# Optimization experiments

Hardware: AMD Instinct MI355X
Metric: run time of the kernel (lower is better)

The kernel has to match this reference:

```python
import jax, jax.numpy as jnp
import numpy as np

NT = 34000      # nodes per type
NTYPES = 3
NMP = 2         # metapaths per node type
E = 300000      # metapath instances per metapath
L = 3           # metapath length
H = 8           # attention heads
D = 64          # hidden_dim (per-head dim)
HD = H * D      # 512
AV = 128        # attn_vec_dim
C = 8           # out_dim (classes)
NTGT = 1000
NLAYERS = 2
N = NTYPES * NT


def _glorot(k, shape, fan_in):
    return jax.random.normal(k, shape, jnp.float32) * (1.0 / np.sqrt(fan_in))


def setup_inputs() -> dict:
    key = jax.random.key(0)
    ks = jax.random.split(key, 24)
    X0 = jax.random.normal(ks[0], (NT, 512), jnp.float32)
    X1 = jax.random.normal(ks[1], (NT, 256), jnp.float32)
    X2 = jax.random.normal(ks[2], (NT, 128), jnp.float32)
    # metapath instances: column 0 is the target node (must be of type i),
    # remaining columns are intermediate nodes of any type
    dst = jax.random.randint(ks[3], (NTYPES, NMP, E), 0, NT) + jnp.arange(NTYPES)[:, None, None] * NT
    mids = jax.random.randint(ks[4], (NTYPES, NMP, E, L - 1), 0, N)
    mp_idx = jnp.concatenate([dst[..., None], mids], axis=-1).astype(jnp.int32)
    target_idx = jax.random.randint(ks[5], (NTGT,), 0, NT).astype(jnp.int32)
    inp = {
        "X0": X0, "X1": X1, "X2": X2,
        # per-type feature transforms (fc_list)
        "fcW0": _glorot(ks[6], (512, D), 512), "fcb0": jnp.zeros((D,), jnp.float32),
        "fcW1": _glorot(ks[7], (256, D), 256), "fcb1": jnp.zeros((D,), jnp.float32),
        "fcW2": _glorot(ks[8], (128, D), 128), "fcb2": jnp.zeros((D,), jnp.float32),
        # GAT-style intra-metapath attention params [layer, type, metapath, H, D]
        "attn1": jax.random.normal(ks[9], (NLAYERS, NTYPES, NMP, H, D), jnp.float32) * 0.1,
        "attn2": jax.random.normal(ks[10], (NLAYERS, NTYPES, NMP, H, D), jnp.float32) * 0.1,
        # inter-metapath attention (fc1 + attention vector q) [layer, type, ...]
        "mpW": _glorot(ks[11], (NLAYERS, NTYPES, HD, AV), HD),
        "mpb": jnp.zeros((NLAYERS, NTYPES, AV), jnp.float32),
        "mpq": jax.random.normal(ks[12], (NLAYERS, NTYPES, AV), jnp.float32) * 0.1,
        # per-layer output fc: in_dim*num_heads -> out_dim
        "lW0": _glorot(ks[13], (HD, D), HD), "lb0": jnp.zeros((D,), jnp.float32),
        "lW1": _glorot(ks[14], (HD, C), HD), "lb1": jnp.zeros((C,), jnp.float32),
        "mp_idx": mp_idx,
        "target_idx": target_idx,
    }
    return inp


def _ctr_layer(h, a1, a2, mpW, mpb, mpq, mp_idx):
    # one MAGNN_nc_layer ctr-ntype pass: gather metapath instances, intra-metapath
    # attention (segment softmax over target node), inter-metapath attention,
    # then scatter per-type results into the shared node tensor (contiguous blocks).
    outs = []
    for i in range(NTYPES):
        per_mp = []
        for p in range(NMP):
            idx = mp_idx[i, p]                      # [E, L]
            feats = h[idx]                          # [E, L, D] irregular gather
            hid = feats.mean(axis=1)                # rnn_type='average' metapath encoding
            dst = idx[:, 0] - i * NT                # local target-node ids
            e = jax.nn.leaky_relu(
                jnp.einsum('ed,hd->eh', feats[:, 0, :], a1[i, p])
                + jnp.einsum('ed,hd->eh', hid, a2[i, p]), 0.2)   # [E, H]
            m = jax.ops.segment_max(e, dst, num_segments=NT)
            ex = jnp.exp(e - m[dst])
            den = jax.ops.segment_sum(ex, dst, num_segments=NT)
            alpha = ex / jnp.maximum(den[dst], 1e-9)             # segment softmax
            out = jax.ops.segment_sum(alpha[:, :, None] * hid[:, None, :], dst,
                                      num_segments=NT)           # [NT, H, D]
            per_mp.append(jax.nn.elu(out.reshape(NT, HD)))
        st = jnp.stack(per_mp)                       # [P, NT, HD]
        s = jnp.tanh(jnp.einsum('pnd,dk->pnk', st, mpW[i]) + mpb[i]).mean(axis=1) @ mpq[i]  # [P]
        beta = jax.nn.softmax(s)
        outs.append(jnp.einsum('p,pnd->nd', beta, st))
    return jnp.concatenate(outs, axis=0)             # scatter back: [N, HD]


def reference(X0, X1, X2, fcW0, fcb0, fcW1, fcb1, fcW2, fcb2,
              attn1, attn2, mpW, mpb, mpq, lW0, lb0, lW1, lb1,
              mp_idx, target_idx):
    # type-masked gather -> per-type linear -> scatter (types are contiguous blocks)
    h = jnp.concatenate([X0 @ fcW0 + fcb0, X1 @ fcW1 + fcb1, X2 @ fcW2 + fcb2], axis=0)
    hm = _ctr_layer(h, attn1[0], attn2[0], mpW[0], mpb[0], mpq[0], mp_idx)
    h = jax.nn.elu(hm @ lW0 + lb0)                   # layer 0: HD -> hidden, ELU
    hm = _ctr_layer(h, attn1[1], attn2[1], mpW[1], mpb[1], mpq[1], mp_idx)
    logits = hm @ lW1 + lb1                          # final layer: HD -> out_dim
    return logits[target_idx]
```

## Files before the change

kernel.cpp:

```cpp
#include <hip/hip_runtime.h>
#include <hip/hip_bf16.h>
#include <math.h>

#define NT 34000
#define NTYPES 3
#define NMP 2
#define NE 300000
#define HH 8
#define DD 64
#define HD 512
#define AV 128
#define NCLS 8
#define NTGT 1000
#define NN (NTYPES*NT)
#define NBLK 133
#define SCBLK 1172
#define TSC (6*SCBLK)
#define TMM (3*532)
#define MAXC 8

typedef short short8 __attribute__((ext_vector_type(8)));
typedef float f32x4 __attribute__((ext_vector_type(4)));

__device__ __forceinline__ short f2bf(float f){
  unsigned u = __float_as_uint(f);
  unsigned r = u + 0x7FFFu + ((u>>16)&1u);
  return (short)(r>>16);
}
__device__ __forceinline__ float bf2f(short s){
  return __uint_as_float(((unsigned)(unsigned short)s)<<16);
}
__device__ __forceinline__ float fast_tanh(float x){
  x = fminf(15.f, fmaxf(-15.f, x));
  float t = __expf(2.f*x);
  return (t-1.f)/(t+1.f);
}

__device__ __forceinline__ void compute_beta(const float* __restrict__ av,
                                             const float* __restrict__ q,
                                             float* b0, float* b1){
  float s0=0.f, s1=0.f;
  #pragma unroll
  for(int c=0;c<32;c++){
    float4 a0=((const float4*)av)[c];
    float4 a1=((const float4*)(av+128))[c];
    float4 qq=((const float4*)q)[c];
    s0 += a0.x*qq.x+a0.y*qq.y+a0.z*qq.z+a0.w*qq.w;
    s1 += a1.x*qq.x+a1.y*qq.y+a1.z*qq.z+a1.w*qq.w;
  }
  s0 /= (float)NT; s1 /= (float)NT;
  float mm=fmaxf(s0,s1);
  float e0=__expf(s0-mm), e1=__expf(s1-mm);
  float d=e0+e1;
  *b0=e0/d; *b1=e1/d;
}

__global__ void k_zero(int* __restrict__ p, int n){
  int i = blockIdx.x*256+threadIdx.x; if(i<n) p[i]=0;
}

__global__ void k_hist(const int* __restrict__ mp, int* __restrict__ counts){
  int e = blockIdx.x*256+threadIdx.x; int g = blockIdx.y;
  if(e>=NE) return;
  int i = g>>1;
  int dst = mp[((size_t)g*NE+e)*3] - i*NT;
  atomicAdd(&counts[g*NT+dst],1);
}

__global__ __launch_bounds__(256) void k_blkred(const int* __restrict__ counts, int* __restrict__ bsum){
  int g=blockIdx.y, blk=blockIdx.x, t=threadIdx.x;
  int idx=blk*256+t;
  int v=(idx<NT)? counts[g*NT+idx]:0;
  #pragma unroll
  for(int off=32;off;off>>=1) v+=__shfl_down(v,off,64);
  __shared__ int sh[4];
  if((t&63)==0) sh[t>>6]=v;
  __syncthreads();
  if(t==0) bsum[g*NBLK+blk]=sh[0]+sh[1]+sh[2]+sh[3];
}

__global__ __launch_bounds__(256) void k_scansums(int* __restrict__ bsum){
  int g=blockIdx.x; int t=threadIdx.x;
  __shared__ int s[256];
  int v=(t<NBLK)? bsum[g*NBLK+t]:0;
  s[t]=v; __syncthreads();
  for(int off=1;off<256;off<<=1){
    int tmp=(t>=off)?s[t-off]:0; __syncthreads();
    s[t]+=tmp; __syncthreads();
  }
  if(t<NBLK) bsum[g*NBLK+t]=s[t]-v;
}

__global__ __launch_bounds__(256) void k_scanapply(int* __restrict__ counts, const int* __restrict__ bsum,
                                                   int* __restrict__ offs){
  int g=blockIdx.y, blk=blockIdx.x, t=threadIdx.x;
  int idx=blk*256+t;
  int v=(idx<NT)? counts[g*NT+idx]:0;
  __shared__ int s[256];
  s[t]=v; __syncthreads();
  for(int off=1;off<256;off<<=1){
    int tmp=(t>=off)?s[t-off]:0; __syncthreads();
    s[t]+=tmp; __syncthreads();
  }
  int excl = s[t]-v + bsum[g*NBLK+blk];
  if(idx<NT){ offs[g*(NT+1)+idx]=excl; counts[g*NT+idx]=0; }
  if(idx==NT-1) offs[g*(NT+1)+NT]=excl+v;
}

__global__ void k_packWall(const float* __restrict__ W0, const float* __restrict__ W1,
                           const float* __restrict__ W2, const float* __restrict__ WL,
                           const float* __restrict__ mpW,
                           short* __restrict__ p0, short* __restrict__ p1,
                           short* __restrict__ p2, short* __restrict__ pL,
                           short* __restrict__ bpk4, float* __restrict__ accv){
  int which = blockIdx.y;
  int tid = blockIdx.x*256+threadIdx.x;
  if(which<4){
    const float* W; short* wpk; int K;
    if(which==0){W=W0;wpk=p0;K=512;}
    else if(which==1){W=W1;wpk=p1;K=256;}
    else if(which==2){W=W2;wpk=p2;K=128;}
    else {W=WL;wpk=pL;K=512;}
    int nk = K>>5;
    int total = nk*256;
    if(tid>=total) return;
    int lane = tid&63; int c=(tid>>6)&3; int kt=tid>>8;
    int col = c*16 + (lane&15);
    int kbase = kt*32 + ((lane>>4)<<3);
    short8 hi, lo;
    #pragma unroll
    for(int j=0;j<8;j++){
      float w = W[(size_t)(kbase+j)*64+col];
      short h = f2bf(w); hi[j]=h;
      lo[j] = f2bf(w - bf2f(h));
    }
    ((short8*)wpk)[tid] = hi;
    ((short8*)wpk)[total+tid] = lo;
  } else {
    if(which==4 && tid<1024) accv[tid]=0.f;
    if(tid>=8192) return;
    const float* W = mpW + (size_t)(which-4)*512*128;
    short* out = bpk4 + (size_t)(which-4)*65536;
    int lane=tid&63; int c=(tid>>6)&7; int t=tid>>9;
    int kbase = t*32 + ((lane>>4)<<3);
    int col = c*16 + (lane&15);
    short8 v;
    #pragma unroll
    for(int jj=0;jj<8;jj++) v[jj]=f2bf(W[(size_t)(kbase+jj)*128+col]);
    ((short8*)out)[tid]=v;
  }
}

__global__ __launch_bounds__(256) void k_scmm(const int* __restrict__ mp, const int* __restrict__ offs,
    int* __restrict__ counts, int2* __restrict__ mids,
    const float* __restrict__ X0, const float* __restrict__ X1, const float* __restrict__ X2,
    const short* __restrict__ wpk0, const short* __restrict__ wpk1, const short* __restrict__ wpk2,
    const float* __restrict__ fb0, const float* __restrict__ fb1, const float* __restrict__ fb2,
    float* __restrict__ Y, short* __restrict__ Yb){
  int bid = blockIdx.x;
  int period = bid/27, r = bid - period*27;
  if(r<22){
    int s = period*22 + r; if(s>=TSC) return;
    int g = s/SCBLK; int e = (s - g*SCBLK)*256 + threadIdx.x;
    if(e>=NE) return;
    int i = g>>1;
    const int* row = mp + ((size_t)g*NE+e)*3;
    int dst = row[0]-i*NT;
    int pos = offs[g*(NT+1)+dst] + atomicAdd(&counts[g*NT+dst],1);
    unsigned long long pk = ((unsigned long long)(unsigned)row[2]<<32) | (unsigned)row[1];
    __builtin_nontemporal_store(pk, (unsigned long long*)&mids[(size_t)g*NE+pos]);
    return;
  }
  int mID = period*5 + (r-22); if(mID>=TMM) return;
  int which = mID/532; int xb = mID - which*532;
  const float* X; const short* wpk; const float* b; int K;
  if(which==0){X=X0;wpk=wpk0;b=fb0;K=512;}
  else if(which==1){X=X1;wpk=wpk1;b=fb1;K=256;}
  else {X=X2;wpk=wpk2;b=fb2;K=128;}
  float* Yw = Y + (size_t)which*NT*64;
  short* Ybw = Yb + (size_t)which*NT*64;
  int wave = threadIdx.x>>6, lane = threadIdx.x&63;
  int row0 = xb*64 + wave*16;
  if(row0>=NT) return;
  int rr = row0 + (lane&15);
  int rc = min(rr, NT-1);
  const float* xr = X + (size_t)rc*K + ((lane>>4)<<3);
  int nk = K>>5;
  const short8* wh = (const short8*)wpk;
  const short8* wl = wh + (size_t)nk*256;
  f32x4 acc[4];
  #pragma unroll
  for(int c=0;c<4;c++) acc[c]=(f32x4){0.f,0.f,0.f,0.f};
  for(int kt=0;kt<nk;kt++){
    float4 f0=*(const float4*)(xr + kt*32);
    float4 f1=*(const float4*)(xr + kt*32 + 4);
    float xs[8]={f0.x,f0.y,f0.z,f0.w,f1.x,f1.y,f1.z,f1.w};
    short8 ah, al;
    #pragma unroll
    for(int j=0;j<8;j++){
      short h=f2bf(xs[j]); ah[j]=h;
      al[j]=f2bf(xs[j]-bf2f(h));
    }
    const short8* whk = wh + (size_t)kt*256 + lane;
    const short8* wlk = wl + (size_t)kt*256 + lane;
    #pragma unroll
    for(int c=0;c<4;c++){
      short8 bh = whk[c*64];
      short8 bl = wlk[c*64];
      acc[c]=__builtin_amdgcn_mfma_f32_16x16x32_bf16(ah,bh,acc[c],0,0,0);
      acc[c]=__builtin_amdgcn_mfma_f32_16x16x32_bf16(al,bh,acc[c],0,0,0);
      acc[c]=__builtin_amdgcn_mfma_f32_16x16x32_bf16(ah,bl,acc[c],0,0,0);
    }
  }
  int rbase = row0 + ((lane>>4)<<2);
  int colb = lane&15;
  #pragma unroll
  for(int c=0;c<4;c++){
    int col = c*16+colb;
    float bb = b[col];
    #pragma unroll
    for(int q=0;q<4;q++){
      int rw = rbase+q;
      if(rw<NT){
        float v = acc[c][q]+bb;
        Yw[(size_t)rw*64+col]=v;
        Ybw[(size_t)rw*64+col]=f2bf(v);
      }
    }
  }
}

__global__ __launch_bounds__(256) void k_mm64fB(const short* __restrict__ Xa, const short* __restrict__ Xb,
               const float* __restrict__ accv_s, const float* __restrict__ q,
               const short* __restrict__ wpk,
               const float* __restrict__ b, float* __restrict__ Y, int rows, int act){
  const int K=512, nk=16;
  float b0, b1;
  compute_beta(accv_s, q, &b0, &b1);
  int wave = threadIdx.x>>6, lane = threadIdx.x&63;
  int row0 = blockIdx.x*64 + wave*16;
  if(row0>=rows) return;
  int r = row0 + (lane&15);
  int rc = min(r, rows-1);
  const short* xra = Xa + (size_t)rc*K + ((lane>>4)<<3);
  const short* xrb = Xb + (size_t)rc*K + ((lane>>4)<<3);
  const short8* wh = (const short8*)wpk;
  const short8* wl = wh + (size_t)nk*256;
  f32x4 acc[4];
  #pragma unroll
  for(int c=0;c<4;c++) acc[c]=(f32x4){0.f,0.f,0.f,0.f};
  for(int kt=0;kt<nk;kt++){
    short8 sa = *(const short8*)(xra + kt*32);
    short8 sb = *(const short8*)(xrb + kt*32);
    short8 ah, al;
    #pragma unroll
    for(int j=0;j<8;j++){
      float x = b0*bf2f(sa[j]) + b1*bf2f(sb[j]);
      short h=f2bf(x); ah[j]=h;
      al[j]=f2bf(x-bf2f(h));
    }
    const short8* whk = wh + (size_t)kt*256 + lane;
    const short8* wlk = wl + (size_t)kt*256 + lane;
    #pragma unroll
    for(int c=0;c<4;c++){
      short8 bh = whk[c*64];
      short8 bl = wlk[c*64];
      acc[c]=__builtin_amdgcn_mfma_f32_16x16x32_bf16(ah,bh,acc[c],0,0,0);
      acc[c]=__builtin_amdgcn_mfma_f32_16x16x32_bf16(al,bh,acc[c],0,0,0);
      acc[c]=__builtin_amdgcn_mfma_f32_16x16x32_bf16(ah,bl,acc[c],0,0,0);
    }
  }
  int rbase = row0 + ((lane>>4)<<2);
  int colb = lane&15;
  #pragma unroll
  for(int c=0;c<4;c++){
    int col = c*16+colb;
    float bb = b[col];
    #pragma unroll
    for(int q=0;q<4;q++){
      int rw = rbase+q;
      if(rw<rows){
        float v = acc[c][q]+bb;
        if(act) v = v>0.f? v : (__expf(v)-1.f);
        Y[(size_t)rw*64+col]=v;
      }
    }
  }
}

__global__ __launch_bounds__(256) void k_pre(const float* __restrict__ h, const float* __restrict__ a1,
              const float* __restrict__ a2, float* __restrict__ ptab, int ngroups,
              short* __restrict__ hbout){
  int node = blockIdx.x*256+threadIdx.x;
  if(node>=NN) return;
  const float* hr = h + (size_t)node*64;
  float4 hv[16];
  #pragma unroll
  for(int q=0;q<16;q++) hv[q]=((const float4*)hr)[q];
  if(hbout){
    short* hp = hbout + (size_t)node*64;
    #pragma unroll
    for(int qq=0;qq<8;qq++){
      float4 a=hv[2*qq], b4=hv[2*qq+1];
      short8 v;
      v[0]=f2bf(a.x); v[1]=f2bf(a.y); v[2]=f2bf(a.z); v[3]=f2bf(a.w);
      v[4]=f2bf(b4.x); v[5]=f2bf(b4.y); v[6]=f2bf(b4.z); v[7]=f2bf(b4.w);
      ((short8*)hp)[qq]=v;
    }
  }
  for(int g=0; g<ngroups; g++){
    const float* A1 = a1 + (size_t)g*512;
    const float* A2 = a2 + (size_t)g*512;
    float out[16];
    #pragma unroll
    for(int o=0;o<8;o++){
      float acc=0.f;
      #pragma unroll
      for(int q=0;q<16;q++){
        float4 w=((const float4*)A1)[o*16+q];
        acc += hv[q].x*w.x+hv[q].y*w.y+hv[q].z*w.z+hv[q].w*w.w;
      }
      out[o]=acc;
    }
    #pragma unroll
    for(int o=0;o<8;o++){
      float acc=0.f;
      #pragma unroll
      for(int q=0;q<16;q++){
        float4 w=((const float4*)A2)[o*16+q];
        acc += hv[q].x*w.x+hv[q].y*w.y+hv[q].z*w.z+hv[q].w*w.w;
      }
      out[8+o]=acc;
    }
    float* dp = ptab + ((size_t)g*NN+node)*16;
    #pragma unroll
    for(int q=0;q<4;q++)
      ((float4*)dp)[q]=make_float4(out[q*4],out[q*4+1],out[q*4+2],out[q*4+3]);
  }
}

__global__ __launch_bounds__(256) void k_seg(const int* __restrict__ offs_all, const float* __restrict__ ptab,
   const int2* __restrict__ mids_all, const float* __restrict__ h, const short* __restrict__ hb,
   short* __restrict__ stb, float* __restrict__ stf, int type, int tobf){
  __shared__ float evw[4][MAXC][64];
  __shared__ float wsh[4][64];
  int wave = threadIdx.x>>6, lane = threadIdx.x&63;
  int n = blockIdx.x*4 + wave;
  if(n>=NT) return;
  int p = blockIdx.y; int g = type*2+p;
  const int* offs = offs_all + (size_t)g*(NT+1);
  const int2* mids_g = mids_all + (size_t)g*NE;
  const float* pt = ptab + (size_t)g*NN*16;
  const unsigned short* hbp = (const unsigned short*)hb;

  int off = offs[n], end = offs[n+1];
  int nc = (end-off+7)>>3;
  const float third = 1.f/3.f;
  int j = lane>>3, hh = lane&7;

  const float* pn = pt + (size_t)(type*NT+n)*16;
  float baseh = pn[hh] + pn[8+hh]*third;

  float m = -1e30f, den = 0.f;
  for(int c=0;c<nc;c++){
    int s = off + c*8 + j;
    float ev = -1e30f;
    if(s<end){
      int2 mm = mids_g[s];
      float q1 = pt[(size_t)mm.x*16 + 8 + hh];
      float q2 = pt[(size_t)mm.y*16 + 8 + hh];
      float e = baseh + (q1+q2)*third;
      ev = e>0.f? e : 0.2f*e;
      float mn = fmaxf(m, ev);
      den = den*__expf(m-mn) + __expf(ev-mn);
      m = mn;
    }
    if(c<MAXC) evw[wave][c][lane]=ev;
  }
  #pragma unroll
  for(int o8=8;o8<=32;o8<<=1){
    float om = __shfl_xor(m, o8, 64);
    float od = __shfl_xor(den, o8, 64);
    float mn = fmaxf(m, om);
    den = den*__expf(m-mn) + od*__expf(om-mn);
    m = mn;
  }
  float invD = 1.f/fmaxf(den, 1e-9f);

  float o[8]={0.f,0.f,0.f,0.f,0.f,0.f,0.f,0.f};
  int c = 0;
  for(int base=off; base<end; base+=8, c++){
    float w;
    if(c<MAXC){
      float ev = evw[wave][c][lane];
      w = __expf(ev-m)*invD;
    } else {
      int s = base+j; w = 0.f;
      if(s<end){
        int2 mm = mids_g[s];
        float q1 = pt[(size_t)mm.x*16 + 8 + hh];
        float q2 = pt[(size_t)mm.y*16 + 8 + hh];
        float e = baseh + (q1+q2)*third;
        float ev2 = e>0.f? e : 0.2f*e;
        w = __expf(ev2-m)*invD;
      }
    }
    wsh[wave][lane] = w;
    int cnt = min(8, end-base);
    for(int k=0;k<cnt;k++){
      int2 mm = mids_g[base+k];
      unsigned ux = hbp[(size_t)mm.x*64+lane];
      unsigned uy = hbp[(size_t)mm.y*64+lane];
      float hvm = __uint_as_float(ux<<16) + __uint_as_float(uy<<16);
      float4 a0 = *(const float4*)&wsh[wave][k*8];
      float4 a1 = *(const float4*)&wsh[wave][k*8+4];
      o[0]+=a0.x*hvm; o[1]+=a0.y*hvm; o[2]+=a0.z*hvm; o[3]+=a0.w*hvm;
      o[4]+=a1.x*hvm; o[5]+=a1.y*hvm; o[6]+=a1.z*hvm; o[7]+=a1.w*hvm;
    }
  }

  float hn = h[((size_t)type*NT+(size_t)n)*64+lane];
  short* stbp = stb + (size_t)p*NT*512 + (size_t)n*512 + lane;
  float* stfp = stf + (size_t)p*NT*512 + (size_t)n*512 + lane;
  #pragma unroll
  for(int q=0;q<8;q++){
    float v = (end>off)? (o[q] + hn)*third : 0.f;
    v = v>0.f? v : (__expf(v)-1.f);
    if(tobf) stbp[q*64] = f2bf(v);
    else     stfp[q*64] = v;
  }
}

__global__ __launch_bounds__(256) void k_tanhmm(const short* __restrict__ stb, const float* __restrict__ stf,
                        int isbf, const short* __restrict__ bpk,
                        const float* __restrict__ bias, float* __restrict__ accv_s){
  __shared__ float red[4][128];
  int wave=threadIdx.x>>6, lane=threadIdx.x&63;
  int p=blockIdx.y;
  int row0 = (blockIdx.x*4+wave)*16;
  int active = (row0<NT);
  int rA = row0 + (lane&15); if(rA>NT-1) rA=NT-1;
  const short* arowb = stb + (size_t)p*NT*512 + (size_t)rA*512 + ((lane>>4)<<3);
  const float* arowf = stf + (size_t)p*NT*512 + (size_t)rA*512 + ((lane>>4)<<3);
  f32x4 acc[8];
  #pragma unroll
  for(int c=0;c<8;c++) acc[c]=(f32x4){0.f,0.f,0.f,0.f};
  const short8* bp = (const short8*)bpk;
  if(active){
    for(int kt=0;kt<16;kt++){
      short8 a;
      if(isbf){
        a = *(const short8*)(arowb + kt*32);
      } else {
        float4 f0 = *(const float4*)(arowf + kt*32);
        float4 f1 = *(const float4*)(arowf + kt*32 + 4);
        a[0]=f2bf(f0.x); a[1]=f2bf(f0.y); a[2]=f2bf(f0.z); a[3]=f2bf(f0.w);
        a[4]=f2bf(f1.x); a[5]=f2bf(f1.y); a[6]=f2bf(f1.z); a[7]=f2bf(f1.w);
      }
      const short8* bk = bp + (size_t)kt*512 + lane;
      #pragma unroll
      for(int c=0;c<8;c++){
        short8 bfr = bk[c*64];
        acc[c]=__builtin_amdgcn_mfma_f32_16x16x32_bf16(a,bfr,acc[c],0,0,0);
      }
    }
  }
  int rbase = row0 + ((lane>>4)<<2);
  int colb = lane&15;
  float sc[8];
  #pragma unroll
  for(int c=0;c<8;c++){
    float s=0.f;
    if(active){
      float bb=bias[c*16+colb];
      #pragma unroll
      for(int r=0;r<4;r++){
        if(rbase+r<NT) s += fast_tanh(acc[c][r]+bb);
      }
    }
    s += __shfl_xor(s,16,64);
    s += __shfl_xor(s,32,64);
    sc[c]=s;
  }
  if(lane<16){
    #pragma unroll
    for(int c=0;c<8;c++) red[wave][c*16+lane]=sc[c];
  }
  __syncthreads();
  if(threadIdx.x<128){
    float t = red[0][threadIdx.x]+red[1][threadIdx.x]+red[2][threadIdx.x]+red[3][threadIdx.x];
    atomicAdd(&accv_s[p*128+threadIdx.x], t);
  }
}

__global__ __launch_bounds__(64) void k_final(const float* __restrict__ st0, const float* __restrict__ st1,
      const float* __restrict__ accv_s, const float* __restrict__ q,
      const float* __restrict__ lW1, const float* __restrict__ lb1,
      const int* __restrict__ tgt, float* __restrict__ out){
  int t=blockIdx.x; int lane=threadIdx.x;
  int row=tgt[t];
  float b0, b1;
  compute_beta(accv_s, q, &b0, &b1);
  float acc[8]={0.f,0.f,0.f,0.f,0.f,0.f,0.f,0.f};
  #pragma unroll
  for(int kk=0;kk<8;kk++){
    int k=kk*64+lane;
    float hm=b0*st0[(size_t)row*512+k]+b1*st1[(size_t)row*512+k];
    const float4* wp=(const float4*)(lW1+(size_t)k*8);
    float4 w0=wp[0], w1=wp[1];
    acc[0]+=hm*w0.x; acc[1]+=hm*w0.y; acc[2]+=hm*w0.z; acc[3]+=hm*w0.w;
    acc[4]+=hm*w1.x; acc[5]+=hm*w1.y; acc[6]+=hm*w1.z; acc[7]+=hm*w1.w;
  }
  #pragma unroll
  for(int c=0;c<8;c++){
    #pragma unroll
    for(int off=32;off>0;off>>=1) acc[c]+=__shfl_xor(acc[c],off,64);
  }
  if(lane<8){
    float v=0.f;
    #pragma unroll
    for(int c=0;c<8;c++) if(lane==c) v=acc[c];
    out[t*8+lane]=v+lb1[lane];
  }
}

extern "C" void kernel_launch(void* const* d_in, const int* in_sizes, int n_in,
                              void* d_out, int out_size, void* d_ws, size_t ws_size,
                              hipStream_t stream) {
  const float* X0=(const float*)d_in[0];
  const float* X1=(const float*)d_in[1];
  const float* X2=(const float*)d_in[2];
  const float* fcW0=(const float*)d_in[3]; const float* fcb0=(const float*)d_in[4];
  const float* fcW1=(const float*)d_in[5]; const float* fcb1=(const float*)d_in[6];
  const float* fcW2=(const float*)d_in[7]; const float* fcb2=(const float*)d_in[8];
  const float* attn1=(const float*)d_in[9];
  const float* attn2=(const float*)d_in[10];
  const float* mpW=(const float*)d_in[11];
  const float* mpb=(const float*)d_in[12];
  const float* mpq=(const float*)d_in[13];
  const float* lW0=(const float*)d_in[14]; const float* lb0=(const float*)d_in[15];
  const float* lW1=(const float*)d_in[16]; const float* lb1=(const float*)d_in[17];
  const int* mp=(const int*)d_in[18];
  const int* tgt=(const int*)d_in[19];
  float* out=(float*)d_out;

  char* ws=(char*)d_ws;
  float* h0   =(float*)(ws+0);
  float* h1   =(float*)(ws+26112000);
  float* ptab =(float*)(ws+52224000);
  int*   offs =(int*  )(ws+91392000);
  int*   counts=(int* )(ws+92208128);
  int2*  mids =(int2* )(ws+100224128);
  short* hb   =(short*)(ws+114624128);
  short* wpk0 =(short*)(ws+127680128);
  short* wpk1 =(short*)(ws+127811200);
  short* wpkL =(short*)(ws+127876736);
  short* wpk2 =(short*)(ws+128007808);
  short* stb  =(short*)(ws+133824128);
  float* stf  =(float*)(ws+133824128);
  short* bpk4 =(short*)(ws+273088128);
  float* accv =(float*)(ws+273612416);
  int*   bsum =(int*  )(ws+133824128);

  dim3 b256(256);
  k_zero<<<dim3((6*NT+255)/256),b256,0,stream>>>(counts,6*NT);
  k_hist<<<dim3((NE+255)/256,6),b256,0,stream>>>(mp,counts);
  k_blkred<<<dim3(NBLK,6),b256,0,stream>>>(counts,bsum);
  k_scansums<<<dim3(6),b256,0,stream>>>(bsum);
  k_scanapply<<<dim3(NBLK,6),b256,0,stream>>>(counts,bsum,offs);

  k_packWall<<<dim3(32,8),b256,0,stream>>>(fcW0,fcW1,fcW2,lW0,mpW,wpk0,wpk1,wpk2,wpkL,bpk4,accv);

  k_scmm<<<dim3(320*27),b256,0,stream>>>(mp,offs,counts,mids,X0,X1,X2,
                                         wpk0,wpk1,wpk2,fcb0,fcb1,fcb2,h0,hb);

  k_pre<<<dim3((NN+255)/256),b256,0,stream>>>(h0,attn1,attn2,ptab,6,(short*)nullptr);
  for(int type=0;type<3;type++){
    k_seg<<<dim3(NT/4,2),b256,0,stream>>>(offs,ptab,mids,h0,hb,stb,stf,type,1);
    k_tanhmm<<<dim3(532,2),b256,0,stream>>>(stb,stf,1,bpk4+(size_t)type*65536,
                                            mpb+(0*3+type)*128,accv+type*256);
    k_mm64fB<<<dim3(532),b256,0,stream>>>(stb,stb+(size_t)NT*512,accv+type*256,mpq+(0*3+type)*128,
                                          wpkL,lb0,h1+(size_t)type*NT*64,NT,1);
  }

  k_pre<<<dim3((NN+255)/256),b256,0,stream>>>(h1,attn1+(size_t)6*512,attn2+(size_t)6*512,ptab,2,hb);
  k_seg<<<dim3(NT/4,2),b256,0,stream>>>(offs,ptab,mids,h1,hb,stb,stf,0,0);
  k_tanhmm<<<dim3(532,2),b256,0,stream>>>(stb,stf,0,bpk4+(size_t)3*65536,
                                          mpb+(1*3+0)*128,accv+3*256);
  k_final<<<dim3(NTGT),dim3(64),0,stream>>>(stf,stf+(size_t)NT*512,accv+3*256,mpq+(1*3+0)*128,
                                            lW1,lb1,tgt,out);
}
```

Before: 1.130 ms.

## Fuse next type's segment aggregation with current type's output matmul

Merges the layer-0 output matmul for one node type and the metapath segment aggregation for the next type into a single launch. Blocks are interleaved so one in every 33 runs the matmul and the rest run the segment work. Double-buffered st buffers (stb0/stb1) let both stages proceed at once. The aim is to overlap the compute-bound MFMA matmul with the gather-heavy segment kernel and to remove some launches, at the cost of a larger workspace footprint and mixed block roles.

```diff
diff --git a/kernel.cpp b/kernel.cpp
--- a/kernel.cpp
+++ b/kernel.cpp
@@ -18,6 +18,7 @@
 #define TSC (6*SCBLK)
 #define TMM (3*532)
 #define MAXC 8
+#define FP 33
 
 typedef short short8 __attribute__((ext_vector_type(8)));
 typedef float f32x4 __attribute__((ext_vector_type(4)));
@@ -230,18 +231,16 @@
   }
 }
 
-__global__ __launch_bounds__(256) void k_mm64fB(const short* __restrict__ Xa, const short* __restrict__ Xb,
+__device__ __forceinline__ void mmB_body(const short* __restrict__ Xa, const short* __restrict__ Xb,
                const float* __restrict__ accv_s, const float* __restrict__ q,
-               const short* __restrict__ wpk,
-               const float* __restrict__ b, float* __restrict__ Y, int rows, int act){
-  const int K=512, nk=16;
+               const short* __restrict__ wpk, const float* __restrict__ b,
+               float* __restrict__ Y, int row0, int lane){
+  const int nk=16, K=512;
   float b0, b1;
   compute_beta(accv_s, q, &b0, &b1);
-  int wave = threadIdx.x>>6, lane = threadIdx.x&63;
-  int row0 = blockIdx.x*64 + wave*16;
-  if(row0>=rows) return;
+  if(row0>=NT) return;
   int r = row0 + (lane&15);
-  int rc = min(r, rows-1);
+  int rc = min(r, NT-1);
   const short* xra = Xa + (size_t)rc*K + ((lane>>4)<<3);
   const short* xrb = Xb + (size_t)rc*K + ((lane>>4)<<3);
   const short8* wh = (const short8*)wpk;
@@ -277,15 +276,22 @@
     int col = c*16+colb;
     float bb = b[col];
     #pragma unroll
-    for(int q=0;q<4;q++){
-      int rw = rbase+q;
-      if(rw<rows){
-        float v = acc[c][q]+bb;
-        if(act) v = v>0.f? v : (__expf(v)-1.f);
+    for(int q2=0;q2<4;q2++){
+      int rw = rbase+q2;
+      if(rw<NT){
+        float v = acc[c][q2]+bb;
+        v = v>0.f? v : (__expf(v)-1.f);
         Y[(size_t)rw*64+col]=v;
       }
     }
   }
+}
+
+__global__ __launch_bounds__(256) void k_mm64fB(const short* __restrict__ Xa, const short* __restrict__ Xb,
+               const float* __restrict__ accv_s, const float* __restrict__ q,
+               const short* __restrict__ wpk, const float* __restrict__ b, float* __restrict__ Y){
+  int wave = threadIdx.x>>6, lane = threadIdx.x&63;
+  mmB_body(Xa,Xb,accv_s,q,wpk,b,Y, blockIdx.x*64+wave*16, lane);
 }
 
 __global__ __launch_bounds__(256) void k_pre(const float* __restrict__ h, const float* __restrict__ a1,
@@ -339,15 +345,13 @@
   }
 }
 
-__global__ __launch_bounds__(256) void k_seg(const int* __restrict__ offs_all, const float* __restrict__ ptab,
-   const int2* __restrict__ mids_all, const float* __restrict__ h, const short* __restrict__ hb,
-   short* __restrict__ stb, float* __restrict__ stf, int type, int tobf){
-  __shared__ float evw[4][MAXC][64];
-  __shared__ float wsh[4][64];
-  int wave = threadIdx.x>>6, lane = threadIdx.x&63;
-  int n = blockIdx.x*4 + wave;
+__device__ __forceinline__ void seg_body(const int* __restrict__ offs_all,
+   const float* __restrict__ ptab, const int2* __restrict__ mids_all,
+   const float* __restrict__ h, const short* __restrict__ hb,
+   short* __restrict__ stb, float* __restrict__ stf, int type, int tobf,
+   int n, int p, float (*__restrict__ evw)[64], float* __restrict__ wsh, int lane){
   if(n>=NT) return;
-  int p = blockIdx.y; int g = type*2+p;
+  int g = type*2+p;
   const int* offs = offs_all + (size_t)g*(NT+1);
   const int2* mids_g = mids_all + (size_t)g*NE;
   const float* pt = ptab + (size_t)g*NN*16;
@@ -375,7 +379,7 @@
       den = den*__expf(m-mn) + __expf(ev-mn);
       m = mn;
     }
-    if(c<MAXC) evw[wave][c][lane]=ev;
+    if(c<MAXC) evw[c][lane]=ev;
   }
   #pragma unroll
   for(int o8=8;o8<=32;o8<<=1){
@@ -392,7 +396,7 @@
   for(int base=off; base<end; base+=8, c++){
     float w;
     if(c<MAXC){
-      float ev = evw[wave][c][lane];
+      float ev = evw[c][lane];
       w = __expf(ev-m)*invD;
     } else {
       int s = base+j; w = 0.f;
@@ -405,29 +409,72 @@
         w = __expf(ev2-m)*invD;
       }
     }
-    wsh[wave][lane] = w;
+    wsh[lane] = w;
     int cnt = min(8, end-base);
     for(int k=0;k<cnt;k++){
       int2 mm = mids_g[base+k];
       unsigned ux = hbp[(size_t)mm.x*64+lane];
       unsigned uy = hbp[(size_t)mm.y*64+lane];
       float hvm = __uint_as_float(ux<<16) + __uint_as_float(uy<<16);
-      float4 a0 = *(const float4*)&wsh[wave][k*8];
-      float4 a1 = *(const float4*)&wsh[wave][k*8+4];
+      float4 a0 = *(const float4*)&wsh[k*8];
+      float4 a1 = *(const float4*)&wsh[k*8+4];
       o[0]+=a0.x*hvm; o[1]+=a0.y*hvm; o[2]+=a0.z*hvm; o[3]+=a0.w*hvm;
       o[4]+=a1.x*hvm; o[5]+=a1.y*hvm; o[6]+=a1.z*hvm; o[7]+=a1.w*hvm;
     }
   }
 
   float hn = h[((size_t)type*NT+(size_t)n)*64+lane];
-  short* stbp = stb + (size_t)p*NT*512 + (size_t)n*512 + lane;
-  float* stfp = stf + (size_t)p*NT*512 + (size_t)n*512 + lane;
-  #pragma unroll
-  for(int q=0;q<8;q++){
-    float v = (end>off)? (o[q] + hn)*third : 0.f;
-    v = v>0.f? v : (__expf(v)-1.f);
-    if(tobf) stbp[q*64] = f2bf(v);
-    else     stfp[q*64] = v;
+  if(tobf){
+    short* stbp = stb + (size_t)p*NT*512 + (size_t)n*512 + lane;
+    #pragma unroll
+    for(int q=0;q<8;q++){
+      float v = (end>off)? (o[q] + hn)*third : 0.f;
+      v = v>0.f? v : (__expf(v)-1.f);
+      stbp[q*64] = f2bf(v);
+    }
+  } else {
+    float* stfp = stf + (size_t)p*NT*512 + (size_t)n*512 + lane;
+    #pragma unroll
+    for(int q=0;q<8;q++){
+      float v = (end>off)? (o[q] + hn)*third : 0.f;
+      v = v>0.f? v : (__expf(v)-1.f);
+      stfp[q*64] = v;
+    }
+  }
+}
+
+__global__ __launch_bounds__(256) void k_seg(const int* __restrict__ offs_all, const float* __restrict__ ptab,
+   const int2* __restrict__ mids_all, const float* __restrict__ h, const short* __restrict__ hb,
+   short* __restrict__ stb, float* __restrict__ stf, int type, int tobf){
+  __shared__ float evw[4][MAXC][64];
+  __shared__ float wsh[4][64];
+  int wave = threadIdx.x>>6, lane = threadIdx.x&63;
+  seg_body(offs_all,ptab,mids_all,h,hb,stb,stf,type,tobf,
+           blockIdx.x*4+wave, blockIdx.y, evw[wave], wsh[wave], lane);
+}
+
+__global__ __launch_bounds__(256) void k_mmseg(
+    const int* __restrict__ offs_all, const float* __restrict__ ptab,
+    const int2* __restrict__ mids_all, const float* __restrict__ h,
+    const short* __restrict__ hb, short* __restrict__ stw, int ts,
+    const short* __restrict__ str, const float* __restrict__ accv_s,
+    const float* __restrict__ q, const short* __restrict__ wpk,
+    const float* __restrict__ b, float* __restrict__ Y){
+  __shared__ float evw[4][MAXC][64];
+  __shared__ float wsh[4][64];
+  int wave = threadIdx.x>>6, lane = threadIdx.x&63;
+  int bid = blockIdx.x;
+  int k33 = bid/FP;
+  if(bid - k33*FP == 0){
+    if(k33>=532) return;
+    mmB_body(str, str+(size_t)NT*512, accv_s, q, wpk, b, Y, k33*64+wave*16, lane);
+  } else {
+    int segID = bid - k33 - 1;
+    if(segID>=17000) return;
+    int p = segID/8500;
+    int nblk = segID - p*8500;
+    seg_body(offs_all,ptab,mids_all,h,hb,stw,(float*)0,ts,1,
+             nblk*4+wave, p, evw[wave], wsh[wave], lane);
   }
 }
 
@@ -556,7 +603,8 @@
   short* wpk1 =(short*)(ws+127811200);
   short* wpkL =(short*)(ws+127876736);
   short* wpk2 =(short*)(ws+128007808);
-  short* stb  =(short*)(ws+133824128);
+  short* stb0 =(short*)(ws+133824128);
+  short* stb1 =(short*)(ws+203456128);
   float* stf  =(float*)(ws+133824128);
   short* bpk4 =(short*)(ws+273088128);
   float* accv =(float*)(ws+273612416);
@@ -575,17 +623,20 @@
                                          wpk0,wpk1,wpk2,fcb0,fcb1,fcb2,h0,hb);
 
   k_pre<<<dim3((NN+255)/256),b256,0,stream>>>(h0,attn1,attn2,ptab,6,(short*)nullptr);
-  for(int type=0;type<3;type++){
-    k_seg<<<dim3(NT/4,2),b256,0,stream>>>(offs,ptab,mids,h0,hb,stb,stf,type,1);
-    k_tanhmm<<<dim3(532,2),b256,0,stream>>>(stb,stf,1,bpk4+(size_t)type*65536,
-                                            mpb+(0*3+type)*128,accv+type*256);
-    k_mm64fB<<<dim3(532),b256,0,stream>>>(stb,stb+(size_t)NT*512,accv+type*256,mpq+(0*3+type)*128,
-                                          wpkL,lb0,h1+(size_t)type*NT*64,NT,1);
-  }
+  k_seg<<<dim3(NT/4,2),b256,0,stream>>>(offs,ptab,mids,h0,hb,stb0,stf,0,1);
+  k_tanhmm<<<dim3(532,2),b256,0,stream>>>(stb0,stf,1,bpk4,mpb,accv);
+  k_mmseg<<<dim3(532*FP),b256,0,stream>>>(offs,ptab,mids,h0,hb,stb1,1,
+          stb0,accv,mpq,wpkL,lb0,h1);
+  k_tanhmm<<<dim3(532,2),b256,0,stream>>>(stb1,stf,1,bpk4+65536,mpb+128,accv+256);
+  k_mmseg<<<dim3(532*FP),b256,0,stream>>>(offs,ptab,mids,h0,hb,stb0,2,
+          stb1,accv+256,mpq+128,wpkL,lb0,h1+(size_t)NT*64);
+  k_tanhmm<<<dim3(532,2),b256,0,stream>>>(stb0,stf,1,bpk4+(size_t)2*65536,mpb+256,accv+512);
+  k_mm64fB<<<dim3(532),b256,0,stream>>>(stb0,stb0+(size_t)NT*512,accv+512,mpq+256,
+          wpkL,lb0,h1+(size_t)2*NT*64);
 
   k_pre<<<dim3((NN+255)/256),b256,0,stream>>>(h1,attn1+(size_t)6*512,attn2+(size_t)6*512,ptab,2,hb);
-  k_seg<<<dim3(NT/4,2),b256,0,stream>>>(offs,ptab,mids,h1,hb,stb,stf,0,0);
-  k_tanhmm<<<dim3(532,2),b256,0,stream>>>(stb,stf,0,bpk4+(size_t)3*65536,
+  k_seg<<<dim3(NT/4,2),b256,0,stream>>>(offs,ptab,mids,h1,hb,stb0,stf,0,0);
+  k_tanhmm<<<dim3(532,2),b256,0,stream>>>(stb0,stf,0,bpk4+(size_t)3*65536,
                                           mpb+(1*3+0)*128,accv+3*256);
   k_final<<<dim3(NTGT),dim3(64),0,stream>>>(stf,stf+(size_t)NT*512,accv+3*256,mpq+(1*3+0)*128,
                                             lW1,lb1,tgt,out);
```

Measured after the change: 1.128 ms. Within noise of the previous version (-0.1%).
